# Performance work log

Hardware: AMD Instinct MI355X
Metric: run time of the kernel (lower is better)

## Reference

```python
import jax, jax.numpy as jnp
import numpy as np
from math import factorial, sqrt

MUL = 128
BATCH = 16384
IRREPS_IN1 = [(MUL, 0, 1), (MUL, 1, -1), (MUL, 2, 1)]   # (mul, l, parity)
IRREPS_IN2 = [(1, 0, 1), (1, 1, -1), (1, 2, 1), (1, 3, -1)]
TARGET = {(0, 1), (1, -1), (2, 1), (3, -1)}               # allowed output (l, parity)


def _su2_cg(j1, m1, j2, m2, j3, m3):
    """Complex Clebsch-Gordan coefficient <j1 m1 j2 m2 | j3 m3> (Racah formula)."""
    if m1 + m2 != m3:
        return 0.0
    f = lambda n: float(factorial(n))
    pref = sqrt((2 * j3 + 1) * f(j1 + j2 - j3) * f(j1 - j2 + j3) * f(-j1 + j2 + j3) / f(j1 + j2 + j3 + 1))
    pref *= sqrt(f(j1 + m1) * f(j1 - m1) * f(j2 + m2) * f(j2 - m2) * f(j3 + m3) * f(j3 - m3))
    s = 0.0
    lo = max(0, j2 - j3 - m1, j1 - j3 + m2)
    hi = min(j1 + j2 - j3, j1 - m1, j2 + m2)
    for k in range(lo, hi + 1):
        s += (-1.0) ** k / (f(k) * f(j1 + j2 - j3 - k) * f(j1 - m1 - k) * f(j2 + m2 - k) * f(j3 - j2 + m1 + k) * f(j3 - j1 - m2 + k))
    return pref * s


def _q(l):
    """Change of basis real SH <- complex SH (e3nn convention, phased)."""
    q = np.zeros((2 * l + 1, 2 * l + 1), dtype=np.complex128)
    for m in range(-l, 0):
        q[l + m, l + abs(m)] = 1.0 / np.sqrt(2)
        q[l + m, l - abs(m)] = -1j / np.sqrt(2)
    q[l, l] = 1.0
    for m in range(1, l + 1):
        q[l + m, l + abs(m)] = (-1) ** m / np.sqrt(2)
        q[l + m, l - abs(m)] = 1j * (-1) ** m / np.sqrt(2)
    return (-1j) ** l * q


def _real_cg(l1, l2, l3):
    """Real-basis CG tensor [2l1+1, 2l2+1, 2l3+1], unit Frobenius norm."""
    Cc = np.zeros((2 * l1 + 1, 2 * l2 + 1, 2 * l3 + 1), dtype=np.complex128)
    for a, m1 in enumerate(range(-l1, l1 + 1)):
        for b, m2 in enumerate(range(-l2, l2 + 1)):
            for c, m3 in enumerate(range(-l3, l3 + 1)):
                Cc[a, b, c] = _su2_cg(l1, m1, l2, m2, l3, m3)
    C = np.einsum('abc,ia,jb,kc->ijk', Cc, np.conj(_q(l1)), np.conj(_q(l2)), _q(l3))
    re, im = np.real(C), np.imag(C)
    C = re if np.linalg.norm(re) >= np.linalg.norm(im) else im  # result is real up to a global phase
    return (C / np.linalg.norm(C)).astype(np.float32)


# enumerate channelwise ('uvu', mul2 == 1) paths allowed by CG selection rules + TARGET filter
PATHS = []
for i, (m1, l1, p1) in enumerate(IRREPS_IN1):
    for j, (m2, l2, p2) in enumerate(IRREPS_IN2):
        for l3 in range(abs(l1 - l2), l1 + l2 + 1):
            if (l3, p1 * p2) in TARGET:
                PATHS.append((i, j, l3))
ORDER = sorted(range(len(PATHS)), key=lambda k: PATHS[k][2])  # stable sort by output l
CG = {(IRREPS_IN1[i][1], IRREPS_IN2[j][1], l3): _real_cg(IRREPS_IN1[i][1], IRREPS_IN2[j][1], l3)
      for (i, j, l3) in PATHS}

OFF1 = np.cumsum([0] + [m * (2 * l + 1) for m, l, _ in IRREPS_IN1])
OFF2 = np.cumsum([0] + [m * (2 * l + 1) for m, l, _ in IRREPS_IN2])
DIM1, DIM2 = int(OFF1[-1]), int(OFF2[-1])          # 1152, 16
WEIGHT_NUMEL = MUL * len(PATHS)                     # 17 * 128 = 2176
DIM_OUT = sum(MUL * (2 * PATHS[k][2] + 1) for k in ORDER)  # 9088


def setup_inputs() -> dict:
    key = jax.random.key(0)
    k1, k2, k3 = jax.random.split(key, 3)
    return {
        'x1': jax.random.normal(k1, (BATCH, DIM1), dtype=jnp.float32),
        'x2': jax.random.normal(k2, (BATCH, DIM2), dtype=jnp.float32),
        'weights': jax.random.normal(k3, (BATCH, WEIGHT_NUMEL), dtype=jnp.float32),
    }


def reference(x1, x2, weights):
    B = x1.shape[0]
    # split mul_ir inputs into per-irrep segments
    x1s = [x1[:, int(OFF1[i]):int(OFF1[i + 1])].reshape(B, m, 2 * l + 1)
           for i, (m, l, _) in enumerate(IRREPS_IN1)]
    x2s = [x2[:, int(OFF2[j]):int(OFF2[j + 1])] for j in range(len(IRREPS_IN2))]  # mul2 == 1
    outs = []
    for k in ORDER:
        i, j, l3 = PATHS[k]
        l1, l2 = IRREPS_IN1[i][1], IRREPS_IN2[j][1]
        C = jnp.asarray(CG[(l1, l2, l3)])                  # [2l1+1, 2l2+1, 2l3+1]
        w = weights[:, k * MUL:(k + 1) * MUL]              # [B, mul] per-edge per-channel weights
        alpha = sqrt((2 * l3 + 1) / MUL)                   # component/element path normalization
        y = jnp.einsum('ijk,bui,bj->buk', C, x1s[i], x2s[j])  # [B, mul, 2l3+1]
        outs.append((alpha * w[:, :, None] * y).reshape(B, MUL * (2 * l3 + 1)))
    return jnp.concatenate(outs, axis=1)  # mul_ir layout, one slot per path, sorted by output l
```

## Files before the change

kernel.cpp:

```cpp
#include <hip/hip_runtime.h>


#define NPATH 17

__device__ const int d_PL1[NPATH]  = {0,0,0,0, 1,1,1,1,1,1, 2,2,2,2,2,2,2};
__device__ const int d_PL2[NPATH]  = {0,1,2,3, 0,1,1,2,2,3, 0,1,1,2,2,3,3};
__device__ const int d_PL3[NPATH]  = {0,1,2,3, 1,0,2,1,3,2, 2,1,3,0,2,1,3};
__device__ const int d_CGOFF[NPATH] = {0,1,10,35,84,93,102,147,192,297,402,427,472,577,602,727,832};
__device__ const int d_X2OFF[NPATH] = {0,1,4,9, 0,1,1,4,4,9, 0,1,1,4,4,9,9};
__device__ const int d_KOFF[NPATH]  = {0,4,8,16,24,36,40,56,68,92,108,136,152,188,196,224,240};
__device__ const int d_KN[NPATH]    = {1,3,5,7, 9,3,15,9,21,15, 25,15,35,5,25,15,35};

__device__ float g_cg[1077];


__device__ double dfactd(int n){ double r=1.0; for(int i=2;i<=n;++i) r *= (double)i; return r; }

__device__ double su2cg(int j1,int m1,int j2,int m2,int j3,int m3){
  if (m1+m2 != m3) return 0.0;
  double pref = sqrt((double)(2*j3+1)*dfactd(j1+j2-j3)*dfactd(j1-j2+j3)*dfactd(-j1+j2+j3)/dfactd(j1+j2+j3+1));
  pref *= sqrt(dfactd(j1+m1)*dfactd(j1-m1)*dfactd(j2+m2)*dfactd(j2-m2)*dfactd(j3+m3)*dfactd(j3-m3));
  int lo = 0;
  if (j2-j3-m1 > lo) lo = j2-j3-m1;
  if (j1-j3+m2 > lo) lo = j1-j3+m2;
  int hi = j1+j2-j3;
  if (j1-m1 < hi) hi = j1-m1;
  if (j2+m2 < hi) hi = j2+m2;
  double s = 0.0;
  for (int k=lo;k<=hi;++k){
    double d = dfactd(k)*dfactd(j1+j2-j3-k)*dfactd(j1-m1-k)*dfactd(j2+m2-k)
             * dfactd(j3-j2+m1+k)*dfactd(j3-j1-m2+k);
    s += ((k&1) ? -1.0 : 1.0)/d;
  }
  return pref*s;
}

struct Cplx { double re, im; };

__device__ int qrow(int l, int r, int* cols, Cplx* vals){
  const double is2 = 0.70710678118654752440;
  int mp = r - l;
  int n;
  double vr[2], vi[2];
  if (mp < 0)      { cols[0]=l-mp; vr[0]=is2;  vi[0]=0.0;  cols[1]=l+mp; vr[1]=0.0; vi[1]=-is2; n=2; }
  else if (mp==0)  { cols[0]=l;    vr[0]=1.0;  vi[0]=0.0;  n=1; }
  else { double sg = (mp&1)? -1.0 : 1.0;
         cols[0]=l+mp; vr[0]=sg*is2; vi[0]=0.0;
         cols[1]=l-mp; vr[1]=0.0;    vi[1]=sg*is2; n=2; }
  int ph = l & 3;
  for (int t=0;t<n;++t){
    double re=vr[t], im=vi[t], nr, ni;
    if      (ph==0){ nr=re;  ni=im;  }
    else if (ph==1){ nr=im;  ni=-re; }
    else if (ph==2){ nr=-re; ni=-im; }
    else           { nr=-im; ni=re;  }
    vals[t].re=nr; vals[t].im=ni;
  }
  return n;
}

__global__ void tp_cg_setup(){
  const int p = blockIdx.x;
  const int l1=d_PL1[p], l2=d_PL2[p], l3=d_PL3[p];
  const int N2=2*l2+1, N3=2*l3+1;
  const int n = (2*l1+1)*N2*N3;
  __shared__ double sre[245], sim[245];
  for (int e=threadIdx.x; e<n; e+=blockDim.x){
    int k = e % N3, rem = e / N3;
    int j = rem % N2, i = rem / N2;
    int ca[2], cb[2], cc[2];
    Cplx va[2], vb[2], vc[2];
    int na=qrow(l1,i,ca,va), nb=qrow(l2,j,cb,vb), nc=qrow(l3,k,cc,vc);
    double ar=0.0, ai=0.0;
    for (int a=0;a<na;++a) for (int b=0;b<nb;++b){
      double r1=va[a].re, i1=-va[a].im;
      double r2=vb[b].re, i2=-vb[b].im;
      double r12 = r1*r2 - i1*i2;
      double i12 = r1*i2 + i1*r2;
      for (int c=0;c<nc;++c){
        double cg = su2cg(l1, ca[a]-l1, l2, cb[b]-l2, l3, cc[c]-l3);
        if (cg != 0.0){
          double r3=vc[c].re, i3=vc[c].im;
          ar += cg*(r12*r3 - i12*i3);
          ai += cg*(r12*i3 + i12*r3);
        }
      }
    }
    sre[e]=ar; sim[e]=ai;
  }
  __syncthreads();
  __shared__ double s_scale;
  __shared__ int s_usere;
  if (threadIdx.x==0){
    double nr=0.0, ni=0.0;
    for (int e=0;e<n;++e){ nr += sre[e]*sre[e]; ni += sim[e]*sim[e]; }
    int ur = (nr >= ni) ? 1 : 0;
    s_usere = ur;
    s_scale = 1.0/sqrt(ur ? nr : ni);
  }
  __syncthreads();
  const int off = d_CGOFF[p];
  for (int e=threadIdx.x; e<n; e+=blockDim.x)
    g_cg[off+e] = (float)((s_usere ? sre[e] : sim[e]) * s_scale);
}


template<int L1, int L3>
__device__ __forceinline__ void path_out(const float* __restrict__ Kp,
                                         const float* __restrict__ xv,
                                         float wa, float* __restrict__ op){
  constexpr int N1 = 2*L1+1, N3 = 2*L3+1;
  float y[N3];
#pragma unroll
  for (int k=0;k<N3;++k) y[k] = 0.0f;
#pragma unroll
  for (int i=0;i<N1;++i){
    const float a = xv[i];
#pragma unroll
    for (int k=0;k<N3;++k) y[k] = fmaf(Kp[i*N3+k], a, y[k]);
  }
#pragma unroll
  for (int k=0;k<N3;++k) op[k] = wa*y[k];
}

__global__ __launch_bounds__(256) void tp_main(const float* __restrict__ x1,
                                               const float* __restrict__ x2,
                                               const float* __restrict__ wts,
                                               float* __restrict__ out){
  __shared__ float sK[276];
  __shared__ __align__(16) float sOut[9088];
  const int tid = threadIdx.x;
  const int t   = tid >> 7;
  const int u   = tid & 127;
  const long long b = blockIdx.x;

  if (tid < 243){
    const float* __restrict__ x2b = x2 + b*16;
    int p=0, rem=tid;
    while (rem >= d_KN[p]) { rem -= d_KN[p]; ++p; }
    const int N3 = 2*d_PL3[p]+1;
    const int N2 = 2*d_PL2[p]+1;
    const int i  = rem / N3;
    const float* __restrict__ C  = g_cg + d_CGOFF[p] + (i*N2)*N3 + (rem % N3);
    const float* __restrict__ xx = x2b + d_X2OFF[p];
    float acc = 0.f;
    for (int j=0;j<N2;++j) acc = fmaf(C[j*N3], xx[j], acc);
    sK[d_KOFF[p] + rem] = acc;
  }
  __syncthreads();

  {
    const float* __restrict__ x1b = x1 + b*1152;
    const float* __restrict__ wb  = wts + b*2176 + u;
    const float* __restrict__ K   = sK;

    const float A0=0.08838834764831845f, A1=0.15309310892394863f,
                A2=0.19764235376052372f, A3=0.23385358667337133f;

    if (t == 0){
      float xv[4];
      xv[0] = x1b[u];
#pragma unroll
      for (int q=0;q<3;++q) xv[1+q] = x1b[128 + 3*u + q];
      path_out<0,0>(K+0,   xv+0, wb[0*128]*A0,  sOut + 0    + u);
      path_out<0,1>(K+4,   xv+0, wb[1*128]*A1,  sOut + 384  + u*3);
      path_out<0,2>(K+8,   xv+0, wb[2*128]*A2,  sOut + 2304 + u*5);
      path_out<0,3>(K+16,  xv+0, wb[3*128]*A3,  sOut + 5504 + u*7);
      path_out<1,1>(K+24,  xv+1, wb[4*128]*A1,  sOut + 768  + u*3);
      path_out<1,0>(K+36,  xv+1, wb[5*128]*A0,  sOut + 128  + u);
      path_out<1,2>(K+40,  xv+1, wb[6*128]*A2,  sOut + 2944 + u*5);
      path_out<1,1>(K+56,  xv+1, wb[7*128]*A1,  sOut + 1152 + u*3);
      path_out<1,3>(K+68,  xv+1, wb[8*128]*A3,  sOut + 6400 + u*7);
      path_out<1,2>(K+92,  xv+1, wb[9*128]*A2,  sOut + 3584 + u*5);
    } else {
      float xv[5];
#pragma unroll
      for (int q=0;q<5;++q) xv[q] = x1b[512 + 5*u + q];
      path_out<2,2>(K+108, xv, wb[10*128]*A2, sOut + 4224 + u*5);
      path_out<2,1>(K+136, xv, wb[11*128]*A1, sOut + 1536 + u*3);
      path_out<2,3>(K+152, xv, wb[12*128]*A3, sOut + 7296 + u*7);
      path_out<2,0>(K+188, xv, wb[13*128]*A0, sOut + 256  + u);
      path_out<2,2>(K+196, xv, wb[14*128]*A2, sOut + 4864 + u*5);
      path_out<2,1>(K+224, xv, wb[15*128]*A1, sOut + 1920 + u*3);
      path_out<2,3>(K+240, xv, wb[16*128]*A3, sOut + 8192 + u*7);
    }
  }
  __syncthreads();

  {
    float4* __restrict__ dst = (float4*)(out + b*9088);
    const float4* __restrict__ src = (const float4*)sOut;
    for (int idx = tid; idx < 2272; idx += 256)
      dst[idx] = src[idx];
  }
}


extern "C" void kernel_launch(void* const* d_in, const int* in_sizes, int n_in,
                              void* d_out, int out_size, void* d_ws, size_t ws_size,
                              hipStream_t stream) {
  const float* x1 = (const float*)d_in[0];
  const float* x2 = (const float*)d_in[1];
  const float* w  = (const float*)d_in[2];
  float* out = (float*)d_out;
  (void)d_ws; (void)ws_size; (void)in_sizes; (void)n_in; (void)out_size;

  tp_cg_setup<<<dim3(NPATH), dim3(256), 0, stream>>>();
  tp_main<<<dim3(16384), dim3(256), 0, stream>>>(x1, x2, w, out);
}
```

Baseline: 188.4 us.

## Compute CG table at compile time, precompute K index map, rebalance path work

Clebsch-Gordan coefficients are now computed with constexpr evaluation and placed in constant memory, which removes the per-call setup kernel launch. A precomputed per-thread map replaces the runtime path search when building the x2-contracted K table. Two l1=2 paths move from the second half-block to the first, evening out FMA work between the two thread groups. The first group now loads the l=2 x1 values as well, which raises its register use slightly.

```diff
diff --git a/kernel.cpp b/kernel.cpp
--- a/kernel.cpp
+++ b/kernel.cpp
@@ -3,106 +3,136 @@
 
 #define NPATH 17
 
-__device__ const int d_PL1[NPATH]  = {0,0,0,0, 1,1,1,1,1,1, 2,2,2,2,2,2,2};
-__device__ const int d_PL2[NPATH]  = {0,1,2,3, 0,1,1,2,2,3, 0,1,1,2,2,3,3};
-__device__ const int d_PL3[NPATH]  = {0,1,2,3, 1,0,2,1,3,2, 2,1,3,0,2,1,3};
-__device__ const int d_CGOFF[NPATH] = {0,1,10,35,84,93,102,147,192,297,402,427,472,577,602,727,832};
-__device__ const int d_X2OFF[NPATH] = {0,1,4,9, 0,1,1,4,4,9, 0,1,1,4,4,9,9};
-__device__ const int d_KOFF[NPATH]  = {0,4,8,16,24,36,40,56,68,92,108,136,152,188,196,224,240};
-__device__ const int d_KN[NPATH]    = {1,3,5,7, 9,3,15,9,21,15, 25,15,35,5,25,15,35};
-
-__device__ float g_cg[1077];
-
-
-__device__ double dfactd(int n){ double r=1.0; for(int i=2;i<=n;++i) r *= (double)i; return r; }
-
-__device__ double su2cg(int j1,int m1,int j2,int m2,int j3,int m3){
+namespace cgc {
+
+constexpr double FT[16] = {1.,1.,2.,6.,24.,120.,720.,5040.,40320.,362880.,
+  3628800.,39916800.,479001600.,6227020800.,87178291200.,1307674368000.};
+
+constexpr double csqrt(double x){
+  if (x <= 0.0) return 0.0;
+  double g = x > 1.0 ? x : 1.0;
+  for (int i=0;i<48;++i) g = 0.5*(g + x/g);
+  return g;
+}
+
+constexpr double su2cg(int j1,int m1,int j2,int m2,int j3,int m3){
   if (m1+m2 != m3) return 0.0;
-  double pref = sqrt((double)(2*j3+1)*dfactd(j1+j2-j3)*dfactd(j1-j2+j3)*dfactd(-j1+j2+j3)/dfactd(j1+j2+j3+1));
-  pref *= sqrt(dfactd(j1+m1)*dfactd(j1-m1)*dfactd(j2+m2)*dfactd(j2-m2)*dfactd(j3+m3)*dfactd(j3-m3));
-  int lo = 0;
-  if (j2-j3-m1 > lo) lo = j2-j3-m1;
-  if (j1-j3+m2 > lo) lo = j1-j3+m2;
-  int hi = j1+j2-j3;
-  if (j1-m1 < hi) hi = j1-m1;
-  if (j2+m2 < hi) hi = j2+m2;
-  double s = 0.0;
+  double pref = csqrt((double)(2*j3+1)*FT[j1+j2-j3]*FT[j1-j2+j3]*FT[-j1+j2+j3]/FT[j1+j2+j3+1]);
+  pref *= csqrt(FT[j1+m1]*FT[j1-m1]*FT[j2+m2]*FT[j2-m2]*FT[j3+m3]*FT[j3-m3]);
+  int lo=0; if (j2-j3-m1>lo) lo=j2-j3-m1; if (j1-j3+m2>lo) lo=j1-j3+m2;
+  int hi=j1+j2-j3; if (j1-m1<hi) hi=j1-m1; if (j2+m2<hi) hi=j2+m2;
+  double s=0.0;
   for (int k=lo;k<=hi;++k){
-    double d = dfactd(k)*dfactd(j1+j2-j3-k)*dfactd(j1-m1-k)*dfactd(j2+m2-k)
-             * dfactd(j3-j2+m1+k)*dfactd(j3-j1-m2+k);
-    s += ((k&1) ? -1.0 : 1.0)/d;
+    double d = FT[k]*FT[j1+j2-j3-k]*FT[j1-m1-k]*FT[j2+m2-k]*FT[j3-j2+m1+k]*FT[j3-j1-m2+k];
+    s += ((k&1)? -1.0:1.0)/d;
   }
   return pref*s;
 }
 
-struct Cplx { double re, im; };
-
-__device__ int qrow(int l, int r, int* cols, Cplx* vals){
+constexpr int qrow(int l, int r, int* cols, double* vr, double* vi){
   const double is2 = 0.70710678118654752440;
   int mp = r - l;
-  int n;
-  double vr[2], vi[2];
-  if (mp < 0)      { cols[0]=l-mp; vr[0]=is2;  vi[0]=0.0;  cols[1]=l+mp; vr[1]=0.0; vi[1]=-is2; n=2; }
-  else if (mp==0)  { cols[0]=l;    vr[0]=1.0;  vi[0]=0.0;  n=1; }
-  else { double sg = (mp&1)? -1.0 : 1.0;
-         cols[0]=l+mp; vr[0]=sg*is2; vi[0]=0.0;
-         cols[1]=l-mp; vr[1]=0.0;    vi[1]=sg*is2; n=2; }
+  int n = 0;
+  double tr[2]={0,0}, ti[2]={0,0};
+  if (mp < 0){ cols[0]=l-mp; tr[0]=is2; ti[0]=0.0; cols[1]=l+mp; tr[1]=0.0; ti[1]=-is2; n=2; }
+  else if (mp==0){ cols[0]=l; tr[0]=1.0; ti[0]=0.0; n=1; }
+  else { double sg=(mp&1)?-1.0:1.0; cols[0]=l+mp; tr[0]=sg*is2; ti[0]=0.0;
+         cols[1]=l-mp; tr[1]=0.0; ti[1]=sg*is2; n=2; }
   int ph = l & 3;
   for (int t=0;t<n;++t){
-    double re=vr[t], im=vi[t], nr, ni;
-    if      (ph==0){ nr=re;  ni=im;  }
-    else if (ph==1){ nr=im;  ni=-re; }
-    else if (ph==2){ nr=-re; ni=-im; }
-    else           { nr=-im; ni=re;  }
-    vals[t].re=nr; vals[t].im=ni;
+    double re=tr[t], im=ti[t], nr=0, ni=0;
+    if (ph==0){ nr=re; ni=im; } else if (ph==1){ nr=im; ni=-re; }
+    else if (ph==2){ nr=-re; ni=-im; } else { nr=-im; ni=re; }
+    vr[t]=nr; vi[t]=ni;
   }
   return n;
 }
 
-__global__ void tp_cg_setup(){
-  const int p = blockIdx.x;
-  const int l1=d_PL1[p], l2=d_PL2[p], l3=d_PL3[p];
-  const int N2=2*l2+1, N3=2*l3+1;
-  const int n = (2*l1+1)*N2*N3;
-  __shared__ double sre[245], sim[245];
-  for (int e=threadIdx.x; e<n; e+=blockDim.x){
-    int k = e % N3, rem = e / N3;
-    int j = rem % N2, i = rem / N2;
-    int ca[2], cb[2], cc[2];
-    Cplx va[2], vb[2], vc[2];
-    int na=qrow(l1,i,ca,va), nb=qrow(l2,j,cb,vb), nc=qrow(l3,k,cc,vc);
-    double ar=0.0, ai=0.0;
-    for (int a=0;a<na;++a) for (int b=0;b<nb;++b){
-      double r1=va[a].re, i1=-va[a].im;
-      double r2=vb[b].re, i2=-vb[b].im;
-      double r12 = r1*r2 - i1*i2;
-      double i12 = r1*i2 + i1*r2;
-      for (int c=0;c<nc;++c){
-        double cg = su2cg(l1, ca[a]-l1, l2, cb[b]-l2, l3, cc[c]-l3);
-        if (cg != 0.0){
-          double r3=vc[c].re, i3=vc[c].im;
-          ar += cg*(r12*r3 - i12*i3);
-          ai += cg*(r12*i3 + i12*r3);
+constexpr int PL1[NPATH] = {0,0,0,0, 1,1,1,1,1,1, 2,2,2,2,2,2,2};
+constexpr int PL2[NPATH] = {0,1,2,3, 0,1,1,2,2,3, 0,1,1,2,2,3,3};
+constexpr int PL3[NPATH] = {0,1,2,3, 1,0,2,1,3,2, 2,1,3,0,2,1,3};
+constexpr int CGOFF[NPATH] = {0,1,10,35,84,93,102,147,192,297,402,427,472,577,602,727,832};
+constexpr int X2OFF[NPATH] = {0,1,4,9, 0,1,1,4,4,9, 0,1,1,4,4,9,9};
+constexpr int KOFF[NPATH]  = {0,4,8,16,24,36,40,56,68,92,108,136,152,188,196,224,240};
+constexpr int KN[NPATH]    = {1,3,5,7, 9,3,15,9,21,15, 25,15,35,5,25,15,35};
+
+struct CGTab { float v[1077]; };
+
+constexpr CGTab make_cg(){
+  CGTab R{};
+  for (int p=0;p<NPATH;++p){
+    const int l1=PL1[p], l2=PL2[p], l3=PL3[p];
+    const int N1=2*l1+1, N2=2*l2+1, N3=2*l3+1;
+    double cc[245] = {};
+    for (int a=0;a<N1;++a) for (int b=0;b<N2;++b){
+      int m1=a-l1, m2=b-l2, m3=m1+m2;
+      if (m3>=-l3 && m3<=l3)
+        cc[(a*N2+b)*N3 + (m3+l3)] = su2cg(l1,m1,l2,m2,l3,m3);
+    }
+    double re[245]={}, im[245]={};
+    for (int i=0;i<N1;++i){
+      int ca[2]={}; double ar[2]={}, ai[2]={};
+      const int na=qrow(l1,i,ca,ar,ai);
+      for (int j=0;j<N2;++j){
+        int cb[2]={}; double br[2]={}, bi[2]={};
+        const int nb=qrow(l2,j,cb,br,bi);
+        for (int k=0;k<N3;++k){
+          int cd[2]={}; double dr[2]={}, di[2]={};
+          const int nd=qrow(l3,k,cd,dr,di);
+          double sr=0, si=0;
+          for (int x=0;x<na;++x) for (int y=0;y<nb;++y){
+            const double r1=ar[x], i1=-ai[x];
+            const double r2=br[y], i2=-bi[y];
+            const double r12 = r1*r2 - i1*i2;
+            const double i12 = r1*i2 + i1*r2;
+            for (int z=0;z<nd;++z){
+              const double cg = cc[(ca[x]*N2+cb[y])*N3 + cd[z]];
+              if (cg != 0.0){
+                sr += cg*(r12*dr[z] - i12*di[z]);
+                si += cg*(r12*di[z] + i12*dr[z]);
+              }
+            }
+          }
+          re[(i*N2+j)*N3+k]=sr; im[(i*N2+j)*N3+k]=si;
         }
       }
     }
-    sre[e]=ar; sim[e]=ai;
-  }
-  __syncthreads();
-  __shared__ double s_scale;
-  __shared__ int s_usere;
-  if (threadIdx.x==0){
-    double nr=0.0, ni=0.0;
-    for (int e=0;e<n;++e){ nr += sre[e]*sre[e]; ni += sim[e]*sim[e]; }
-    int ur = (nr >= ni) ? 1 : 0;
-    s_usere = ur;
-    s_scale = 1.0/sqrt(ur ? nr : ni);
-  }
-  __syncthreads();
-  const int off = d_CGOFF[p];
-  for (int e=threadIdx.x; e<n; e+=blockDim.x)
-    g_cg[off+e] = (float)((s_usere ? sre[e] : sim[e]) * s_scale);
-}
+    const int n = N1*N2*N3;
+    double nr=0, ni=0;
+    for (int e=0;e<n;++e){ nr += re[e]*re[e]; ni += im[e]*im[e]; }
+    const bool usere = (nr >= ni);
+    const double sc = 1.0 / csqrt(usere ? nr : ni);
+    for (int e=0;e<n;++e)
+      R.v[CGOFF[p]+e] = (float)((usere ? re[e] : im[e]) * sc);
+  }
+  return R;
+}
+
+struct EMap { unsigned short cgbase, dst; unsigned char stride, cnt, x2off, pad; };
+struct EMaps { EMap m[243]; };
+constexpr EMaps make_emaps(){
+  EMaps M{};
+  int e=0;
+  for (int p=0;p<NPATH;++p){
+    const int l2=PL2[p], l3=PL3[p];
+    const int N2=2*l2+1, N3=2*l3+1;
+    for (int rem=0; rem<KN[p]; ++rem, ++e){
+      const int i = rem / N3, k = rem % N3;
+      M.m[e].cgbase = (unsigned short)(CGOFF[p] + i*N2*N3 + k);
+      M.m[e].dst    = (unsigned short)(KOFF[p] + rem);
+      M.m[e].stride = (unsigned char)N3;
+      M.m[e].cnt    = (unsigned char)N2;
+      M.m[e].x2off  = (unsigned char)X2OFF[p];
+      M.m[e].pad    = 0;
+    }
+  }
+  return M;
+}
+
+}
+
+__device__ __constant__ cgc::CGTab c_cg  = cgc::make_cg();
+__device__ __constant__ cgc::EMaps c_map = cgc::make_emaps();
 
 
 template<int L1, int L3>
@@ -135,17 +165,12 @@
   const long long b = blockIdx.x;
 
   if (tid < 243){
-    const float* __restrict__ x2b = x2 + b*16;
-    int p=0, rem=tid;
-    while (rem >= d_KN[p]) { rem -= d_KN[p]; ++p; }
-    const int N3 = 2*d_PL3[p]+1;
-    const int N2 = 2*d_PL2[p]+1;
-    const int i  = rem / N3;
-    const float* __restrict__ C  = g_cg + d_CGOFF[p] + (i*N2)*N3 + (rem % N3);
-    const float* __restrict__ xx = x2b + d_X2OFF[p];
+    const cgc::EMap m = c_map.m[tid];
+    const float* __restrict__ C  = c_cg.v + m.cgbase;
+    const float* __restrict__ xx = x2 + b*16 + m.x2off;
     float acc = 0.f;
-    for (int j=0;j<N2;++j) acc = fmaf(C[j*N3], xx[j], acc);
-    sK[d_KOFF[p] + rem] = acc;
+    for (int j=0;j<m.cnt;++j) acc = fmaf(C[j*m.stride], xx[j], acc);
+    sK[m.dst] = acc;
   }
   __syncthreads();
 
@@ -158,31 +183,34 @@
                 A2=0.19764235376052372f, A3=0.23385358667337133f;
 
     if (t == 0){
-      float xv[4];
-      xv[0] = x1b[u];
-#pragma unroll
-      for (int q=0;q<3;++q) xv[1+q] = x1b[128 + 3*u + q];
-      path_out<0,0>(K+0,   xv+0, wb[0*128]*A0,  sOut + 0    + u);
-      path_out<0,1>(K+4,   xv+0, wb[1*128]*A1,  sOut + 384  + u*3);
-      path_out<0,2>(K+8,   xv+0, wb[2*128]*A2,  sOut + 2304 + u*5);
-      path_out<0,3>(K+16,  xv+0, wb[3*128]*A3,  sOut + 5504 + u*7);
-      path_out<1,1>(K+24,  xv+1, wb[4*128]*A1,  sOut + 768  + u*3);
-      path_out<1,0>(K+36,  xv+1, wb[5*128]*A0,  sOut + 128  + u);
-      path_out<1,2>(K+40,  xv+1, wb[6*128]*A2,  sOut + 2944 + u*5);
-      path_out<1,1>(K+56,  xv+1, wb[7*128]*A1,  sOut + 1152 + u*3);
-      path_out<1,3>(K+68,  xv+1, wb[8*128]*A3,  sOut + 6400 + u*7);
-      path_out<1,2>(K+92,  xv+1, wb[9*128]*A2,  sOut + 3584 + u*5);
+      float xa[4];
+      xa[0] = x1b[u];
+#pragma unroll
+      for (int q=0;q<3;++q) xa[1+q] = x1b[128 + 3*u + q];
+      float xc[5];
+#pragma unroll
+      for (int q=0;q<5;++q) xc[q] = x1b[512 + 5*u + q];
+      path_out<0,0>(K+0,   xa,   wb[0*128]*A0,  sOut + 0    + u);
+      path_out<0,1>(K+4,   xa,   wb[1*128]*A1,  sOut + 384  + u*3);
+      path_out<0,2>(K+8,   xa,   wb[2*128]*A2,  sOut + 2304 + u*5);
+      path_out<0,3>(K+16,  xa,   wb[3*128]*A3,  sOut + 5504 + u*7);
+      path_out<1,1>(K+24,  xa+1, wb[4*128]*A1,  sOut + 768  + u*3);
+      path_out<1,0>(K+36,  xa+1, wb[5*128]*A0,  sOut + 128  + u);
+      path_out<1,2>(K+40,  xa+1, wb[6*128]*A2,  sOut + 2944 + u*5);
+      path_out<1,1>(K+56,  xa+1, wb[7*128]*A1,  sOut + 1152 + u*3);
+      path_out<1,3>(K+68,  xa+1, wb[8*128]*A3,  sOut + 6400 + u*7);
+      path_out<1,2>(K+92,  xa+1, wb[9*128]*A2,  sOut + 3584 + u*5);
+      path_out<2,0>(K+188, xc,   wb[13*128]*A0, sOut + 256  + u);
+      path_out<2,2>(K+196, xc,   wb[14*128]*A2, sOut + 4864 + u*5);
     } else {
-      float xv[5];
-#pragma unroll
-      for (int q=0;q<5;++q) xv[q] = x1b[512 + 5*u + q];
-      path_out<2,2>(K+108, xv, wb[10*128]*A2, sOut + 4224 + u*5);
-      path_out<2,1>(K+136, xv, wb[11*128]*A1, sOut + 1536 + u*3);
-      path_out<2,3>(K+152, xv, wb[12*128]*A3, sOut + 7296 + u*7);
-      path_out<2,0>(K+188, xv, wb[13*128]*A0, sOut + 256  + u);
-      path_out<2,2>(K+196, xv, wb[14*128]*A2, sOut + 4864 + u*5);
-      path_out<2,1>(K+224, xv, wb[15*128]*A1, sOut + 1920 + u*3);
-      path_out<2,3>(K+240, xv, wb[16*128]*A3, sOut + 8192 + u*7);
+      float xc[5];
+#pragma unroll
+      for (int q=0;q<5;++q) xc[q] = x1b[512 + 5*u + q];
+      path_out<2,2>(K+108, xc, wb[10*128]*A2, sOut + 4224 + u*5);
+      path_out<2,1>(K+136, xc, wb[11*128]*A1, sOut + 1536 + u*3);
+      path_out<2,3>(K+152, xc, wb[12*128]*A3, sOut + 7296 + u*7);
+      path_out<2,1>(K+224, xc, wb[15*128]*A1, sOut + 1920 + u*3);
+      path_out<2,3>(K+240, xc, wb[16*128]*A3, sOut + 8192 + u*7);
     }
   }
   __syncthreads();
@@ -205,6 +233,5 @@
   float* out = (float*)d_out;
   (void)d_ws; (void)ws_size; (void)in_sizes; (void)n_in; (void)out_size;
 
-  tp_cg_setup<<<dim3(NPATH), dim3(256), 0, stream>>>();
   tp_main<<<dim3(16384), dim3(256), 0, stream>>>(x1, x2, w, out);
 }
```

Measured after the change: 167.2 us. -11.3%, faster.
